# Performance work log

Hardware: AMD Instinct MI355X
Metric: run time of the kernel (lower is better)

## Reference

```python
import jax, jax.numpy as jnp
import numpy as np

N_DETS = 8192
DEG = 64
E = N_DETS * DEG
NUM_BLOCKS = 8
SHORTCUT = 128   # shortcutDim
RED = 32         # reducedDim
INNER = 64       # blockInnerDim = 2*32
PW_RAW = 9
PW_HID = 256
PW_OUT = 32


def setup_inputs() -> dict:
    key = jax.random.key(0)
    ks = jax.random.split(key, 24)
    # valid boxes: x2 > x1, y2 > y1
    x1 = jax.random.uniform(ks[0], (N_DETS, 1), jnp.float32, 0.0, 1000.0)
    y1 = jax.random.uniform(ks[1], (N_DETS, 1), jnp.float32, 0.0, 1000.0)
    w = jax.random.uniform(ks[2], (N_DETS, 1), jnp.float32, 8.0, 128.0)
    h = jax.random.uniform(ks[3], (N_DETS, 1), jnp.float32, 8.0, 128.0)
    dtBoxes = jnp.concatenate([x1, y1, x1 + w, y1 + h], axis=1)
    detScores = jax.random.uniform(ks[4], (N_DETS, 1), jnp.float32)
    # every detection has DEG neighbors (first one is itself) -> no empty segments
    cIdxs = jnp.repeat(jnp.arange(N_DETS, dtype=jnp.int32), DEG)
    nIdxs = jax.random.randint(ks[5], (E,), 0, N_DETS, dtype=jnp.int32)
    nIdxs = nIdxs.at[::DEG].set(jnp.arange(N_DETS, dtype=jnp.int32))
    detFeatures = jnp.zeros((N_DETS, SHORTCUT), jnp.float32)

    def lin(k, fan_in, fan_out):
        b = 1.0 / np.sqrt(fan_in)
        return jax.random.uniform(k, (fan_in, fan_out), jnp.float32, -b, b)

    inp = dict(detScores=detScores, dtBoxes=dtBoxes, detFeatures=detFeatures,
               cIdxs=cIdxs, nIdxs=nIdxs)
    # pairwise feature generator MLP: 9 -> 256 -> 256 -> 32 (ReLU after each)
    inp['pw_W0'] = lin(ks[6], PW_RAW, PW_HID); inp['pw_b0'] = jnp.zeros((PW_HID,), jnp.float32)
    inp['pw_W1'] = lin(ks[7], PW_HID, PW_HID); inp['pw_b1'] = jnp.zeros((PW_HID,), jnp.float32)
    inp['pw_W2'] = lin(ks[8], PW_HID, PW_OUT); inp['pw_b2'] = jnp.zeros((PW_OUT,), jnp.float32)
    # per-block params, stacked over NUM_BLOCKS
    B = NUM_BLOCKS
    inp['blk_fc1_W'] = jnp.stack([lin(jax.random.fold_in(ks[9], i), SHORTCUT, RED) for i in range(B)])
    inp['blk_fc1_b'] = jnp.zeros((B, RED), jnp.float32)
    inp['blk_pw1_W'] = jnp.stack([lin(jax.random.fold_in(ks[10], i), 3 * RED, INNER) for i in range(B)])
    inp['blk_pw1_b'] = jnp.zeros((B, INNER), jnp.float32)
    inp['blk_pw2_W'] = jnp.stack([lin(jax.random.fold_in(ks[11], i), INNER, INNER) for i in range(B)])
    inp['blk_pw2_b'] = jnp.zeros((B, INNER), jnp.float32)
    inp['blk_post_W'] = jnp.stack([jnp.stack([lin(jax.random.fold_in(ks[12], 2 * i + j), INNER, INNER) for j in range(2)]) for i in range(B)])
    inp['blk_post_b'] = jnp.zeros((B, 2, INNER), jnp.float32)
    inp['blk_out_W'] = jnp.stack([lin(jax.random.fold_in(ks[13], i), INNER, SHORTCUT) for i in range(B)])
    inp['blk_out_b'] = jnp.zeros((B, SHORTCUT), jnp.float32)
    return inp


def _pairwise_raw(detScores, dtBoxes, cIdxs, nIdxs):
    # box data (getBoxData)
    x1, y1, x2, y2 = (dtBoxes[:, i:i + 1] for i in range(4))
    w, h = x2 - x1, y2 - y1
    area = w * h
    c, n = cIdxs, nIdxs
    # per-edge IoU (dt_dt_iou gathered at (c,n))
    ix = jnp.maximum(0.0, jnp.minimum(x2[c], x2[n]) - jnp.maximum(x1[c], x1[n]))
    iy = jnp.maximum(0.0, jnp.minimum(y2[c], y2[n]) - jnp.maximum(y1[c], y1[n]))
    inter = ix * iy
    iou = inter / (area[c] + area[n] - inter)
    c_w, c_h, n_w, n_h = w[c], h[c], w[n], h[n]
    c_scale = (c_w + c_h) / 2.0
    c_cx, c_cy = x1[c] + c_w / 2.0, y1[c] + c_h / 2.0
    n_cx, n_cy = x1[n] + n_w / 2.0, y1[n] + n_h / 2.0
    x_dist = n_cx - c_cx
    y_dist = n_cy - c_cy
    l2_dist = jnp.sqrt(x_dist ** 2 + y_dist ** 2) / c_scale
    x_dist = x_dist / c_scale
    y_dist = y_dist / c_scale
    log2 = jnp.log(jnp.float32(2.0))
    w_diff = jnp.log(n_w / c_w) / log2
    h_diff = jnp.log(n_h / c_h) / log2
    aspect_diff = (jnp.log(n_w / n_h) - jnp.log(c_w / c_h)) / log2
    return jnp.concatenate([detScores[c], detScores[n], iou, x_dist, y_dist,
                            l2_dist, w_diff, h_diff, aspect_diff], axis=1)  # [E,9]


def reference(detScores, dtBoxes, detFeatures, pw_W0, pw_b0, pw_W1, pw_b1,
              pw_W2, pw_b2, blk_fc1_W, blk_fc1_b, blk_pw1_W, blk_pw1_b,
              blk_pw2_W, blk_pw2_b, blk_post_W, blk_post_b, blk_out_W,
              blk_out_b, cIdxs, nIdxs):
    relu = jax.nn.relu
    numDets = detFeatures.shape[0]
    raw = _pairwise_raw(detScores, dtBoxes, cIdxs, nIdxs)
    pf = relu(raw @ pw_W0 + pw_b0)
    pf = relu(pf @ pw_W1 + pw_b1)
    pairFeatures = relu(pf @ pw_W2 + pw_b2)  # [E,32]

    f = detFeatures
    for i in range(blk_fc1_W.shape[0]):
        f1 = relu(f @ blk_fc1_W[i] + blk_fc1_b[i])                       # [N,32]
        comb = jnp.concatenate([pairFeatures, f1[cIdxs], f1[nIdxs]], 1)  # [E,96]
        comb = relu(comb @ blk_pw1_W[i] + blk_pw1_b[i])
        comb = relu(comb @ blk_pw2_W[i] + blk_pw2_b[i])                  # [E,64]
        pooled = jax.ops.segment_max(comb, cIdxs, num_segments=numDets)  # [N,64]
        pooled = relu(pooled @ blk_post_W[i, 0] + blk_post_b[i, 0])
        pooled = relu(pooled @ blk_post_W[i, 1] + blk_post_b[i, 1])
        f = relu(f + pooled @ blk_out_W[i] + blk_out_b[i])               # [N,128]
    return f
```

## Files before the change

kernel.cpp:

```cpp
#include <hip/hip_runtime.h>
#include <hip/hip_bf16.h>

typedef _Float16 half8 __attribute__((ext_vector_type(8)));
typedef __fp16 fp16x2 __attribute__((ext_vector_type(2)));
typedef float f32x4 __attribute__((ext_vector_type(4)));

#define N_DETS 8192

#define OFF_W0P   0
#define OFF_W1P   8192
#define OFF_W2P   73728
#define OFF_FC1P  81920
#define OFF_PW1P  114688
#define OFF_PW2P  163840
#define OFF_POSTP 196608
#define OFF_OUTP  262144
#define OFF_F1A   327680
#define OFF_F1B   589824
#define OFF_PFP   1114112
#define OFF_FBUF_BYTES 35782656


__device__ inline f32x4 mfma16(half8 a, half8 b, f32x4 c){
  return __builtin_amdgcn_mfma_f32_16x16x32_f16(a, b, c, 0, 0, 0);
}
__device__ inline half8 ldg8(const _Float16* p){ return *(const half8*)p; }

__device__ inline unsigned pkrtz(float a, float b){
  union { fp16x2 h; unsigned u; } x;
  x.h = __builtin_amdgcn_cvt_pkrtz(a, b);
  return x.u;
}
__device__ inline unsigned hmax2u(unsigned a, unsigned b){
  unsigned r;
  asm("v_pk_max_f16 %0, %1, %2" : "=v"(r) : "v"(a), "v"(b));
  return r;
}
__device__ inline unsigned hadd2u(unsigned a, unsigned b){
  unsigned r;
  asm("v_pk_add_f16 %0, %1, %2" : "=v"(r) : "v"(a), "v"(b));
  return r;
}

__device__ inline half8 cvtpack(f32x4 A, f32x4 B){
  union { unsigned w[4]; half8 h; } r;
  r.w[0] = pkrtz(A[0], A[1]); r.w[1] = pkrtz(A[2], A[3]);
  r.w[2] = pkrtz(B[0], B[1]); r.w[3] = pkrtz(B[2], B[3]);
  return r.h;
}

__device__ inline void packB(const float* W, int Ksrc, int Nn, _Float16* dst, int sig){
  int ns = (Ksrc + 31) >> 5;
  int t = sig / (ns * 64);
  int rem = sig - t * ns * 64;
  int s = rem >> 6;
  int l = rem & 63;
  int col = t * 16 + (l & 15);
  int g = l >> 4;
  half8 v;
#pragma unroll
  for (int j = 0; j < 8; ++j){
    int k = s*32 + ((j>>2)<<4) + g*4 + (j&3);
    v[j] = (_Float16)((k < Ksrc) ? W[k * Nn + col] : 0.f);
  }
  *(half8*)(dst + sig * 8) = v;
}

__device__ inline void packW0(const float* W, const float* bias, _Float16* dst, int sig){
  int t = sig >> 6, l = sig & 63;
  int col = t * 16 + (l & 15);
  int g = l >> 4;
  half8 v;
#pragma unroll
  for (int j = 0; j < 8; ++j){
    int k = ((j>>2)<<4) + g*4 + (j&3);
    float x = 0.f;
    if (k < 9) x = W[k * 256 + col];
    else if (k == 9) x = bias[col];
    v[j] = (_Float16)x;
  }
  *(half8*)(dst + sig * 8) = v;
}

__global__ __launch_bounds__(256) void kPrep(const float* pwW0, const float* pwb0,
    const float* pwW1, const float* pwW2,
    const float* fc1W, const float* pw1W, const float* pw2W, const float* postW, const float* outW,
    _Float16* wsh){
  int sig = blockIdx.x * 256 + threadIdx.x;
  if (sig < 1024){ packW0(pwW0, pwb0, wsh + OFF_W0P, sig); return; }
  sig -= 1024;
  if (sig < 8192){ packB(pwW1, 256, 256, wsh + OFF_W1P, sig); return; }
  sig -= 8192;
  if (sig < 1024){ packB(pwW2, 256, 32, wsh + OFF_W2P, sig); return; }
  sig -= 1024;
  int i = sig / 3840;
  int q = sig - i * 3840;
  if (q < 512){ packB(fc1W + i*4096, 128, 32, wsh + OFF_FC1P + i*4096, q); return; }
  q -= 512;
  if (q < 768){ packB(pw1W + i*6144, 96, 64, wsh + OFF_PW1P + i*6144, q); return; }
  q -= 768;
  if (q < 512){ packB(pw2W + i*4096, 64, 64, wsh + OFF_PW2P + i*4096, q); return; }
  q -= 512;
  if (q < 512){ packB(postW + i*8192, 64, 64, wsh + OFF_POSTP + i*8192, q); return; }
  q -= 512;
  if (q < 512){ packB(postW + i*8192 + 4096, 64, 64, wsh + OFF_POSTP + i*8192 + 4096, q); return; }
  q -= 512;
  packB(outW + i*8192, 64, 128, wsh + OFF_OUTP + i*8192, q);
}

__global__ __launch_bounds__(512) void kP(const float* scores, const float* boxes,
    const int* cI, const int* nI, const float* b1, const float* b2,
    const _Float16* W0p, const _Float16* W1p, const _Float16* W2p, _Float16* pfp){
  __shared__ __align__(16) _Float16 sbuf[2][8192];
  __shared__ __align__(16) _Float16 rawp[8192];
  int tid = threadIdx.x;
  int lane = tid & 63, wave = tid >> 6;
  const f32x4 fz = {0.f, 0.f, 0.f, 0.f};

  half8 w0ld[2], s0ld[2];
#pragma unroll
  for (int it = 0; it < 2; ++it){
    w0ld[it] = ldg8(W0p + it*4096 + tid*8);
    s0ld[it] = ldg8(W1p + it*4096 + tid*8);
  }
  {
    half8 z = {0,0,0,0,0,0,0,0};
#pragma unroll
    for (int it = 0; it < 2; ++it) *(half8*)(rawp + it*4096 + tid*8) = z;
  }
  __syncthreads();
  if (tid < 256){
    int e = blockIdx.x*256 + tid;
    int c = cI[e], n = nI[e];
    float cx1 = boxes[c*4+0], cy1 = boxes[c*4+1], cx2 = boxes[c*4+2], cy2 = boxes[c*4+3];
    float nx1 = boxes[n*4+0], ny1 = boxes[n*4+1], nx2 = boxes[n*4+2], ny2 = boxes[n*4+3];
    float cw = cx2-cx1, ch = cy2-cy1, nw = nx2-nx1, nh = ny2-ny1;
    float ca = cw*ch, na = nw*nh;
    float ix = fmaxf(fminf(cx2,nx2) - fmaxf(cx1,nx1), 0.f);
    float iy = fmaxf(fminf(cy2,ny2) - fmaxf(cy1,ny1), 0.f);
    float inter = ix*iy;
    float iou = inter / (ca + na - inter);
    float cs = (cw + ch) * 0.5f;
    float xd = (nx1 + nw*0.5f) - (cx1 + cw*0.5f);
    float yd = (ny1 + nh*0.5f) - (cy1 + ch*0.5f);
    float l2 = sqrtf(xd*xd + yd*yd) / cs;
    float wd = log2f(nw/cw), hd = log2f(nh/ch);
    float ad = log2f(nw/nh) - log2f(cw/ch);
    float rv[10] = {scores[c], scores[n], iou, xd/cs, yd/cs, l2, wd, hd, ad, 1.0f};
    int base = (tid >> 4) * 512;
    int r = tid & 15;
#pragma unroll
    for (int k = 0; k < 10; ++k)
      rawp[base + (((k>>2)&3)*16 + r)*8 + (k&3)] = (_Float16)rv[k];
  }
#pragma unroll
  for (int it = 0; it < 2; ++it){
    *(half8*)(&sbuf[0][0] + it*4096 + tid*8) = w0ld[it];
    *(half8*)(&sbuf[1][0] + it*4096 + tid*8) = s0ld[it];
  }
  __syncthreads();

  half8 h0f[2][8];
#pragma unroll
  for (int et = 0; et < 2; ++et){
    half8 braw = *(const half8*)(rawp + ((wave*2+et)*64 + lane)*8);
#pragma unroll
    for (int mp = 0; mp < 8; ++mp){
      f32x4 a = mfma16(*(const half8*)(&sbuf[0][0] + (2*mp)*512   + lane*8), braw, fz);
      f32x4 b = mfma16(*(const half8*)(&sbuf[0][0] + (2*mp+1)*512 + lane*8), braw, fz);
#pragma unroll
      for (int r = 0; r < 4; ++r){ a[r] = fmaxf(a[r], 0.f); b[r] = fmaxf(b[r], 0.f); }
      h0f[et][mp] = cvtpack(a, b);
    }
  }
  __syncthreads();

  int q = lane >> 4;
  f32x4 apf[2][2];
  apf[0][0] = fz; apf[0][1] = fz; apf[1][0] = fz; apf[1][1] = fz;
  for (int mp = 0; mp < 8; ++mp){
    const _Float16* cur = &sbuf[(mp+1)&1][0];
    half8 stg[2];
    if (mp < 7){
#pragma unroll
      for (int it = 0; it < 2; ++it)
        stg[it] = ldg8(W1p + (mp+1)*8192 + it*4096 + tid*8);
    }
    f32x4 acc[2][2];
    acc[0][0] = fz; acc[0][1] = fz; acc[1][0] = fz; acc[1][1] = fz;
#pragma unroll
    for (int s = 0; s < 8; ++s){
      half8 A0 = *(const half8*)(cur + s*512       + lane*8);
      half8 A1 = *(const half8*)(cur + (8+s)*512   + lane*8);
#pragma unroll
      for (int et = 0; et < 2; ++et){
        acc[et][0] = mfma16(A0, h0f[et][s], acc[et][0]);
        acc[et][1] = mfma16(A1, h0f[et][s], acc[et][1]);
      }
    }
    f32x4 bv0 = *(const f32x4*)(b1 + mp*32 + q*4);
    f32x4 bv1 = *(const f32x4*)(b1 + mp*32 + 16 + q*4);
    half8 w2a = ldg8(W2p + mp*512 + lane*8);
    half8 w2b = ldg8(W2p + (8+mp)*512 + lane*8);
#pragma unroll
    for (int et = 0; et < 2; ++et){
      f32x4 ra, rb;
#pragma unroll
      for (int r = 0; r < 4; ++r){
        ra[r] = fmaxf(acc[et][0][r] + bv0[r], 0.f);
        rb[r] = fmaxf(acc[et][1][r] + bv1[r], 0.f);
      }
      half8 h1f = cvtpack(ra, rb);
      apf[et][0] = mfma16(w2a, h1f, apf[et][0]);
      apf[et][1] = mfma16(w2b, h1f, apf[et][1]);
    }
    if (mp < 7){
      _Float16* nxt = &sbuf[mp&1][0];
#pragma unroll
      for (int it = 0; it < 2; ++it)
        *(half8*)(nxt + it*4096 + tid*8) = stg[it];
    }
    __syncthreads();
  }
  f32x4 c0 = *(const f32x4*)(b2 + q*4);
  f32x4 c1 = *(const f32x4*)(b2 + 16 + q*4);
#pragma unroll
  for (int et = 0; et < 2; ++et){
    f32x4 ra, rb;
#pragma unroll
    for (int r = 0; r < 4; ++r){
      ra[r] = fmaxf(apf[et][0][r] + c0[r], 0.f);
      rb[r] = fmaxf(apf[et][1][r] + c1[r], 0.f);
    }
    half8 pf = cvtpack(ra, rb);
    *(half8*)(pfp + (blockIdx.x*16 + wave*2 + et)*512 + lane*8) = pf;
  }
}

__global__ __launch_bounds__(256) void kF1(const float* detF, const _Float16* fc1p,
    const float* fb, _Float16* f1G){
  int lane = threadIdx.x & 63, wave = threadIdx.x >> 6;
  int q = lane >> 4, e = lane & 15;
  int det = (blockIdx.x * 4 + wave) * 16 + e;
  const f32x4 fz = {0.f, 0.f, 0.f, 0.f};
  half8 ff[4];
#pragma unroll
  for (int s = 0; s < 4; ++s){
    const float* p = detF + det*128 + s*32 + q*4;
    f32x4 x0 = *(const f32x4*)(p);
    f32x4 x1 = *(const f32x4*)(p + 16);
    union { unsigned w[4]; half8 h; } u;
    u.w[0] = pkrtz(x0[0], x0[1]); u.w[1] = pkrtz(x0[2], x0[3]);
    u.w[2] = pkrtz(x1[0], x1[1]); u.w[3] = pkrtz(x1[2], x1[3]);
    ff[s] = u.h;
  }
#pragma unroll
  for (int m = 0; m < 2; ++m){
    f32x4 a = fz;
#pragma unroll
    for (int s = 0; s < 4; ++s)
      a = mfma16(ldg8(fc1p + (m*4+s)*512 + lane*8), ff[s], a);
    f32x4 bv = *(const f32x4*)(fb + m*16 + q*4);
    unsigned u0 = pkrtz(fmaxf(a[0]+bv[0],0.f), fmaxf(a[1]+bv[1],0.f));
    unsigned u1 = pkrtz(fmaxf(a[2]+bv[2],0.f), fmaxf(a[3]+bv[3],0.f));
    *(unsigned*)(f1G + det*32 + q*8 + m*4)     = u0;
    *(unsigned*)(f1G + det*32 + q*8 + m*4 + 2) = u1;
  }
}

__global__ __launch_bounds__(256) void kBlk(const _Float16* pfp, const _Float16* f1in,
    _Float16* f1out, const int* nI, const _Float16* pw1p, const _Float16* pw2p,
    const _Float16* post0p, const _Float16* post1p, const _Float16* outp, const _Float16* fc1pn,
    const float* bb1, const float* bb2, const float* pb0, const float* pb1, const float* ob,
    const float* fbn, const float* fin, float* fout, int doF1){
  __shared__ __align__(16) _Float16 poolS[1024];
  int tid = threadIdx.x, lane = tid & 63, wave = tid >> 6;
  int q = lane >> 4, e = lane & 15;
  int base = blockIdx.x * 16;
  const f32x4 fz = {0.f, 0.f, 0.f, 0.f};

  half8 aW1[4][3], aW2[4][2];
  f32x4 b1v[4];
  unsigned b2p[8];
#pragma unroll
  for (int m = 0; m < 4; ++m){
#pragma unroll
    for (int k = 0; k < 3; ++k) aW1[m][k] = ldg8(pw1p + (m*3+k)*512 + lane*8);
#pragma unroll
    for (int k = 0; k < 2; ++k) aW2[m][k] = ldg8(pw2p + (m*2+k)*512 + lane*8);
    b1v[m] = *(const f32x4*)(bb1 + m*16 + q*4);
    b2p[m*2+0] = pkrtz(bb2[m*16 + q*4 + 0], bb2[m*16 + q*4 + 1]);
    b2p[m*2+1] = pkrtz(bb2[m*16 + q*4 + 2], bb2[m*16 + q*4 + 3]);
  }

  for (int dd = 0; dd < 4; ++dd){
    int d = wave*4 + dd;
    int det = base + d;
    half8 Bc = ldg8(f1in + det*32 + q*8);
    int nn[4];
#pragma unroll
    for (int et = 0; et < 4; ++et) nn[et] = nI[det*64 + et*16 + e];
    half8 Bpf[4], Bn[4];
#pragma unroll
    for (int et = 0; et < 4; ++et){
      Bpf[et] = ldg8(pfp + (det*4+et)*512 + lane*8);
      Bn[et]  = ldg8(f1in + nn[et]*32 + q*8);
    }
    f32x4 bcb[4];
#pragma unroll
    for (int m = 0; m < 4; ++m){
      f32x4 dc = mfma16(aW1[m][1], Bc, fz);
#pragma unroll
      for (int r = 0; r < 4; ++r) bcb[m][r] = dc[r] + b1v[m][r];
    }
    unsigned pm[8];
#pragma unroll
    for (int i = 0; i < 8; ++i) pm[i] = 0xFC00FC00u;
#pragma unroll
    for (int et = 0; et < 4; ++et){
      f32x4 acc[4];
#pragma unroll
      for (int m = 0; m < 4; ++m){
        acc[m] = mfma16(aW1[m][0], Bpf[et], fz);
        acc[m] = mfma16(aW1[m][2], Bn[et], acc[m]);
      }
      f32x4 r0, r1, r2, r3;
#pragma unroll
      for (int r = 0; r < 4; ++r){
        r0[r] = fmaxf(acc[0][r] + bcb[0][r], 0.f);
        r1[r] = fmaxf(acc[1][r] + bcb[1][r], 0.f);
        r2[r] = fmaxf(acc[2][r] + bcb[2][r], 0.f);
        r3[r] = fmaxf(acc[3][r] + bcb[3][r], 0.f);
      }
      half8 h1a = cvtpack(r0, r1);
      half8 h1b = cvtpack(r2, r3);
      f32x4 a2[4];
#pragma unroll
      for (int m = 0; m < 4; ++m){
        a2[m] = mfma16(aW2[m][0], h1a, fz);
        a2[m] = mfma16(aW2[m][1], h1b, a2[m]);
      }
      union { half8 h; unsigned w[4]; } uA, uB;
      uA.h = cvtpack(a2[0], a2[1]);
      uB.h = cvtpack(a2[2], a2[3]);
#pragma unroll
      for (int i = 0; i < 4; ++i){
        pm[i]   = hmax2u(pm[i],   uA.w[i]);
        pm[4+i] = hmax2u(pm[4+i], uB.w[i]);
      }
    }
#pragma unroll
    for (int s = 1; s <= 8; s <<= 1){
#pragma unroll
      for (int i = 0; i < 8; ++i)
        pm[i] = hmax2u(pm[i], __shfl_xor(pm[i], s));
    }
#pragma unroll
    for (int i = 0; i < 8; ++i)
      pm[i] = hmax2u(hadd2u(pm[i], b2p[i]), 0u);
    if (e == 0){
      union { unsigned w[4]; half8 h; } o0, o1;
#pragma unroll
      for (int i = 0; i < 4; ++i){ o0.w[i] = pm[i]; o1.w[i] = pm[4+i]; }
      *(half8*)(poolS + d*32 + q*8)       = o0.h;
      *(half8*)(poolS + 512 + d*32 + q*8) = o1.h;
    }
  }
  __syncthreads();

  half8 Bp0 = *(const half8*)(poolS + e*32 + q*8);
  half8 Bp1 = *(const half8*)(poolS + 512 + e*32 + q*8);
  int det = base + e;
  f32x4 t0[4];
#pragma unroll
  for (int m = 0; m < 4; ++m){
    f32x4 a = mfma16(ldg8(post0p + (m*2)*512   + lane*8), Bp0, fz);
    a = mfma16(ldg8(post0p + (m*2+1)*512 + lane*8), Bp1, a);
    f32x4 bv = *(const f32x4*)(pb0 + m*16 + q*4);
#pragma unroll
    for (int r = 0; r < 4; ++r) t0[m][r] = fmaxf(a[r] + bv[r], 0.f);
  }
  half8 p1a = cvtpack(t0[0], t0[1]);
  half8 p1b = cvtpack(t0[2], t0[3]);
#pragma unroll
  for (int m = 0; m < 4; ++m){
    f32x4 a = mfma16(ldg8(post1p + (m*2)*512   + lane*8), p1a, fz);
    a = mfma16(ldg8(post1p + (m*2+1)*512 + lane*8), p1b, a);
    f32x4 bv = *(const f32x4*)(pb1 + m*16 + q*4);
#pragma unroll
    for (int r = 0; r < 4; ++r) t0[m][r] = fmaxf(a[r] + bv[r], 0.f);
  }
  half8 p2a = cvtpack(t0[0], t0[1]);
  half8 p2b = cvtpack(t0[2], t0[3]);
  f32x4 fr[8];
#pragma unroll
  for (int m = 0; m < 8; ++m){
    f32x4 a = mfma16(ldg8(outp + (m*2)*512   + lane*8), p2a, fz);
    a = mfma16(ldg8(outp + (m*2+1)*512 + lane*8), p2b, a);
    f32x4 bv = *(const f32x4*)(ob + m*16 + q*4);
    f32x4 fv = *(const f32x4*)(fin + det*128 + m*16 + q*4);
#pragma unroll
    for (int r = 0; r < 4; ++r) fr[m][r] = fmaxf(fv[r] + a[r] + bv[r], 0.f);
  }
#pragma unroll
  for (int mm = 0; mm < 2; ++mm){
    int m = wave*2 + mm;
    *(f32x4*)(fout + det*128 + m*16 + q*4) = fr[m];
  }
  if (doF1 && wave == 0){
    half8 ff[4];
#pragma unroll
    for (int s = 0; s < 4; ++s) ff[s] = cvtpack(fr[2*s], fr[2*s+1]);
#pragma unroll
    for (int m = 0; m < 2; ++m){
      f32x4 a = fz;
#pragma unroll
      for (int s = 0; s < 4; ++s)
        a = mfma16(ldg8(fc1pn + (m*4+s)*512 + lane*8), ff[s], a);
      f32x4 bv = *(const f32x4*)(fbn + m*16 + q*4);
      unsigned u0 = pkrtz(fmaxf(a[0]+bv[0],0.f), fmaxf(a[1]+bv[1],0.f));
      unsigned u1 = pkrtz(fmaxf(a[2]+bv[2],0.f), fmaxf(a[3]+bv[3],0.f));
      *(unsigned*)(f1out + det*32 + q*8 + m*4)     = u0;
      *(unsigned*)(f1out + det*32 + q*8 + m*4 + 2) = u1;
    }
  }
}

extern "C" void kernel_launch(void* const* d_in, const int* in_sizes, int n_in,
                              void* d_out, int out_size, void* d_ws, size_t ws_size,
                              hipStream_t stream){
  const float* detScores   = (const float*)d_in[0];
  const float* dtBoxes     = (const float*)d_in[1];
  const float* detFeatures = (const float*)d_in[2];
  const int*   cI          = (const int*)d_in[3];
  const int*   nI          = (const int*)d_in[4];
  const float* pwW0 = (const float*)d_in[5];
  const float* pwb0 = (const float*)d_in[6];
  const float* pwW1 = (const float*)d_in[7];
  const float* pwb1 = (const float*)d_in[8];
  const float* pwW2 = (const float*)d_in[9];
  const float* pwb2 = (const float*)d_in[10];
  const float* fc1W = (const float*)d_in[11];
  const float* fc1b = (const float*)d_in[12];
  const float* pw1W = (const float*)d_in[13];
  const float* pw1b = (const float*)d_in[14];
  const float* pw2W = (const float*)d_in[15];
  const float* pw2b = (const float*)d_in[16];
  const float* postW = (const float*)d_in[17];
  const float* postb = (const float*)d_in[18];
  const float* outW  = (const float*)d_in[19];
  const float* outb  = (const float*)d_in[20];

  _Float16* wsh  = (_Float16*)d_ws;
  float*    fbuf = (float*)((char*)d_ws + OFF_FBUF_BYTES);
  _Float16* f1A  = wsh + OFF_F1A;
  _Float16* f1B  = wsh + OFF_F1B;
  _Float16* pfp  = wsh + OFF_PFP;

  kPrep<<<160, 256, 0, stream>>>(pwW0, pwb0, pwW1, pwW2, fc1W, pw1W, pw2W, postW, outW, wsh);
  kF1<<<128, 256, 0, stream>>>(detFeatures, wsh + OFF_FC1P, fc1b, f1A);
  kP<<<2048, 512, 0, stream>>>(detScores, dtBoxes, cI, nI, pwb1, pwb2,
      wsh + OFF_W0P, wsh + OFF_W1P, wsh + OFF_W2P, pfp);

  for (int i = 0; i < 8; ++i){
    int last = (i == 7);
    _Float16* fin1  = (i & 1) ? f1B : f1A;
    _Float16* fout1 = (i & 1) ? f1A : f1B;
    kBlk<<<512, 256, 0, stream>>>(pfp, fin1, fout1, nI,
        wsh + OFF_PW1P + i*6144, wsh + OFF_PW2P + i*4096,
        wsh + OFF_POSTP + i*8192, wsh + OFF_POSTP + i*8192 + 4096, wsh + OFF_OUTP + i*8192,
        wsh + OFF_FC1P + ((i+1) & 7)*4096,
        pw1b + i*64, pw2b + i*64, postb + i*128, postb + i*128 + 64, outb + i*128,
        fc1b + ((i+1) & 7)*32,
        (i == 0) ? detFeatures : fbuf, last ? (float*)d_out : fbuf, last ? 0 : 1);
  }
}
```

Before: 286.3 us.

## Halve kP block size to 256 threads and apply bias+ReLU in packed fp16

The pairwise MLP kernel now runs 4096 blocks of 256 threads, each covering 128 edges instead of 256. Each block still loads the full W0 and W1 tiles into shared memory, so total weight staging traffic doubles. The aim is more resident blocks per CU and less synchronisation stall from the many __syncthreads in the W1 pipeline. Bias-add and ReLU move from fp32 per-element ops to packed fp16 add/max after conversion, which cuts VALU work but rounds before the bias is added.

Result: no change. 283.5 us (-0.9%).

```diff
diff --git a/kernel.cpp b/kernel.cpp
--- a/kernel.cpp
+++ b/kernel.cpp
@@ -46,6 +46,22 @@
   union { unsigned w[4]; half8 h; } r;
   r.w[0] = pkrtz(A[0], A[1]); r.w[1] = pkrtz(A[2], A[3]);
   r.w[2] = pkrtz(B[0], B[1]); r.w[3] = pkrtz(B[2], B[3]);
+  return r.h;
+}
+__device__ inline half8 cvtpackbr(f32x4 A, f32x4 B, const unsigned* pb){
+  union { unsigned w[4]; half8 h; } r;
+  r.w[0] = pkrtz(A[0], A[1]); r.w[1] = pkrtz(A[2], A[3]);
+  r.w[2] = pkrtz(B[0], B[1]); r.w[3] = pkrtz(B[2], B[3]);
+#pragma unroll
+  for (int i = 0; i < 4; ++i) r.w[i] = hmax2u(hadd2u(r.w[i], pb[i]), 0u);
+  return r.h;
+}
+__device__ inline half8 cvtpackr(f32x4 A, f32x4 B){
+  union { unsigned w[4]; half8 h; } r;
+  r.w[0] = pkrtz(A[0], A[1]); r.w[1] = pkrtz(A[2], A[3]);
+  r.w[2] = pkrtz(B[0], B[1]); r.w[3] = pkrtz(B[2], B[3]);
+#pragma unroll
+  for (int i = 0; i < 4; ++i) r.w[i] = hmax2u(r.w[i], 0u);
   return r.h;
 }
 
@@ -108,29 +124,29 @@
   packB(outW + i*8192, 64, 128, wsh + OFF_OUTP + i*8192, q);
 }
 
-__global__ __launch_bounds__(512) void kP(const float* scores, const float* boxes,
+__global__ __launch_bounds__(256) void kP(const float* scores, const float* boxes,
     const int* cI, const int* nI, const float* b1, const float* b2,
     const _Float16* W0p, const _Float16* W1p, const _Float16* W2p, _Float16* pfp){
   __shared__ __align__(16) _Float16 sbuf[2][8192];
-  __shared__ __align__(16) _Float16 rawp[8192];
+  __shared__ __align__(16) _Float16 rawp[4096];
   int tid = threadIdx.x;
   int lane = tid & 63, wave = tid >> 6;
   const f32x4 fz = {0.f, 0.f, 0.f, 0.f};
 
-  half8 w0ld[2], s0ld[2];
-#pragma unroll
-  for (int it = 0; it < 2; ++it){
-    w0ld[it] = ldg8(W0p + it*4096 + tid*8);
-    s0ld[it] = ldg8(W1p + it*4096 + tid*8);
+  half8 w0ld[4], s0ld[4];
+#pragma unroll
+  for (int it = 0; it < 4; ++it){
+    w0ld[it] = ldg8(W0p + it*2048 + tid*8);
+    s0ld[it] = ldg8(W1p + it*2048 + tid*8);
   }
   {
     half8 z = {0,0,0,0,0,0,0,0};
 #pragma unroll
-    for (int it = 0; it < 2; ++it) *(half8*)(rawp + it*4096 + tid*8) = z;
+    for (int it = 0; it < 2; ++it) *(half8*)(rawp + it*2048 + tid*8) = z;
   }
   __syncthreads();
-  if (tid < 256){
-    int e = blockIdx.x*256 + tid;
+  if (tid < 128){
+    int e = blockIdx.x*128 + tid;
     int c = cI[e], n = nI[e];
     float cx1 = boxes[c*4+0], cy1 = boxes[c*4+1], cx2 = boxes[c*4+2], cy2 = boxes[c*4+3];
     float nx1 = boxes[n*4+0], ny1 = boxes[n*4+1], nx2 = boxes[n*4+2], ny2 = boxes[n*4+3];
@@ -154,9 +170,9 @@
       rawp[base + (((k>>2)&3)*16 + r)*8 + (k&3)] = (_Float16)rv[k];
   }
 #pragma unroll
-  for (int it = 0; it < 2; ++it){
-    *(half8*)(&sbuf[0][0] + it*4096 + tid*8) = w0ld[it];
-    *(half8*)(&sbuf[1][0] + it*4096 + tid*8) = s0ld[it];
+  for (int it = 0; it < 4; ++it){
+    *(half8*)(&sbuf[0][0] + it*2048 + tid*8) = w0ld[it];
+    *(half8*)(&sbuf[1][0] + it*2048 + tid*8) = s0ld[it];
   }
   __syncthreads();
 
@@ -168,9 +184,7 @@
     for (int mp = 0; mp < 8; ++mp){
       f32x4 a = mfma16(*(const half8*)(&sbuf[0][0] + (2*mp)*512   + lane*8), braw, fz);
       f32x4 b = mfma16(*(const half8*)(&sbuf[0][0] + (2*mp+1)*512 + lane*8), braw, fz);
-#pragma unroll
-      for (int r = 0; r < 4; ++r){ a[r] = fmaxf(a[r], 0.f); b[r] = fmaxf(b[r], 0.f); }
-      h0f[et][mp] = cvtpack(a, b);
+      h0f[et][mp] = cvtpackr(a, b);
     }
   }
   __syncthreads();
@@ -180,11 +194,11 @@
   apf[0][0] = fz; apf[0][1] = fz; apf[1][0] = fz; apf[1][1] = fz;
   for (int mp = 0; mp < 8; ++mp){
     const _Float16* cur = &sbuf[(mp+1)&1][0];
-    half8 stg[2];
+    half8 stg[4];
     if (mp < 7){
 #pragma unroll
-      for (int it = 0; it < 2; ++it)
-        stg[it] = ldg8(W1p + (mp+1)*8192 + it*4096 + tid*8);
+      for (int it = 0; it < 4; ++it)
+        stg[it] = ldg8(W1p + (mp+1)*8192 + it*2048 + tid*8);
     }
     f32x4 acc[2][2];
     acc[0][0] = fz; acc[0][1] = fz; acc[1][0] = fz; acc[1][1] = fz;
@@ -198,42 +212,36 @@
         acc[et][1] = mfma16(A1, h0f[et][s], acc[et][1]);
       }
     }
-    f32x4 bv0 = *(const f32x4*)(b1 + mp*32 + q*4);
-    f32x4 bv1 = *(const f32x4*)(b1 + mp*32 + 16 + q*4);
+    unsigned pb[4];
+    pb[0] = pkrtz(b1[mp*32 + q*4 + 0], b1[mp*32 + q*4 + 1]);
+    pb[1] = pkrtz(b1[mp*32 + q*4 + 2], b1[mp*32 + q*4 + 3]);
+    pb[2] = pkrtz(b1[mp*32 + 16 + q*4 + 0], b1[mp*32 + 16 + q*4 + 1]);
+    pb[3] = pkrtz(b1[mp*32 + 16 + q*4 + 2], b1[mp*32 + 16 + q*4 + 3]);
     half8 w2a = ldg8(W2p + mp*512 + lane*8);
     half8 w2b = ldg8(W2p + (8+mp)*512 + lane*8);
 #pragma unroll
     for (int et = 0; et < 2; ++et){
-      f32x4 ra, rb;
-#pragma unroll
-      for (int r = 0; r < 4; ++r){
-        ra[r] = fmaxf(acc[et][0][r] + bv0[r], 0.f);
-        rb[r] = fmaxf(acc[et][1][r] + bv1[r], 0.f);
-      }
-      half8 h1f = cvtpack(ra, rb);
+      half8 h1f = cvtpackbr(acc[et][0], acc[et][1], pb);
       apf[et][0] = mfma16(w2a, h1f, apf[et][0]);
       apf[et][1] = mfma16(w2b, h1f, apf[et][1]);
     }
     if (mp < 7){
       _Float16* nxt = &sbuf[mp&1][0];
 #pragma unroll
-      for (int it = 0; it < 2; ++it)
-        *(half8*)(nxt + it*4096 + tid*8) = stg[it];
+      for (int it = 0; it < 4; ++it)
+        *(half8*)(nxt + it*2048 + tid*8) = stg[it];
     }
     __syncthreads();
   }
-  f32x4 c0 = *(const f32x4*)(b2 + q*4);
-  f32x4 c1 = *(const f32x4*)(b2 + 16 + q*4);
+  unsigned pc[4];
+  pc[0] = pkrtz(b2[q*4 + 0], b2[q*4 + 1]);
+  pc[1] = pkrtz(b2[q*4 + 2], b2[q*4 + 3]);
+  pc[2] = pkrtz(b2[16 + q*4 + 0], b2[16 + q*4 + 1]);
+  pc[3] = pkrtz(b2[16 + q*4 + 2], b2[16 + q*4 + 3]);
 #pragma unroll
   for (int et = 0; et < 2; ++et){
-    f32x4 ra, rb;
-#pragma unroll
-    for (int r = 0; r < 4; ++r){
-      ra[r] = fmaxf(apf[et][0][r] + c0[r], 0.f);
-      rb[r] = fmaxf(apf[et][1][r] + c1[r], 0.f);
-    }
-    half8 pf = cvtpack(ra, rb);
-    *(half8*)(pfp + (blockIdx.x*16 + wave*2 + et)*512 + lane*8) = pf;
+    half8 pf = cvtpackbr(apf[et][0], apf[et][1], pc);
+    *(half8*)(pfp + (blockIdx.x*8 + wave*2 + et)*512 + lane*8) = pf;
   }
 }
 
@@ -459,7 +467,7 @@
 
   kPrep<<<160, 256, 0, stream>>>(pwW0, pwb0, pwW1, pwW2, fc1W, pw1W, pw2W, postW, outW, wsh);
   kF1<<<128, 256, 0, stream>>>(detFeatures, wsh + OFF_FC1P, fc1b, f1A);
-  kP<<<2048, 512, 0, stream>>>(detScores, dtBoxes, cI, nI, pwb1, pwb2,
+  kP<<<4096, 256, 0, stream>>>(detScores, dtBoxes, cI, nI, pwb1, pwb2,
       wsh + OFF_W0P, wsh + OFF_W1P, wsh + OFF_W2P, pfp);
 
   for (int i = 0; i < 8; ++i){
```
